# Kernel tuning notes

Hardware: AMD Instinct MI355X
Metric: run time of the kernel (lower is better)

The kernel has to match this reference:

```python
import jax, jax.numpy as jnp
import numpy as np

B = 16384
NEG = 10
V = 100000
E = 128

def setup_inputs() -> dict:
    key = jax.random.key(0)
    k1, k2, k3, k4, k5 = jax.random.split(key, 5)
    input_word = jax.random.randint(k1, (B,), 0, V)
    context_word = jax.random.randint(k2, (B,), 0, V)
    noise_words = jax.random.randint(k3, (B * NEG,), 0, V)
    # torch init: uniform_(-1, 1)
    W_in = jax.random.uniform(k4, (V, E), jnp.float32, -1.0, 1.0)
    W_ctx = jax.random.uniform(k5, (V, E), jnp.float32, -1.0, 1.0)
    return {"input_word": input_word, "context_word": context_word,
            "noise_words": noise_words, "W_in": W_in, "W_ctx": W_ctx}

def reference(input_word, context_word, noise_words, W_in, W_ctx):
    center = W_in[input_word]               # [B, E]
    ctx = W_ctx[context_word]               # [B, E]
    # positive score: per-example dot product
    out_loss = jax.nn.log_sigmoid(jnp.einsum('be,be->b', ctx, center))  # [B]
    noise = W_ctx[noise_words].reshape(B, NEG, E)                       # [B, NEG, E]
    # negative scores: -u_k . v_c
    neg_scores = -jnp.einsum('bke,be->bk', noise, center)               # [B, NEG]
    noise_loss = jax.nn.log_sigmoid(neg_scores).sum(axis=1)             # [B]
    return -(out_loss + noise_loss).mean()
```

## Files before the change

### kernel.cpp

```cpp
#include <hip/hip_runtime.h>
#include <hip/hip_bf16.h>

constexpr int kB   = 16384;
constexpr int kNeg = 10;
constexpr int kE   = 128;
constexpr int kWavesPerBlock = 4;
constexpr int kPairsPerWave  = 2;
constexpr int kBlocks = kB / (2 * kWavesPerBlock * kPairsPerWave);

__device__ __forceinline__ float log_sigmoid(float x) {
    return fminf(x, 0.0f) - log1pf(expf(-fabsf(x)));
}

__global__ __launch_bounds__(256) void w2v_loss_kernel(
    const int*   __restrict__ input_word,
    const int*   __restrict__ context_word,
    const int*   __restrict__ noise_words,
    const float* __restrict__ W_in,
    const float* __restrict__ W_ctx,
    float*       __restrict__ partials)
{
    const int lane = threadIdx.x & 63;
    const int wave = threadIdx.x >> 6;
    const int half = lane >> 5;
    const int l32  = lane & 31;

    const int wave_global = blockIdx.x * kWavesPerBlock + wave;
    const int pair0 = wave_global * kPairsPerWave;

    float acc = 0.0f;

    for (int p = 0; p < kPairsPerWave; ++p) {
        const int b = (pair0 + p) * 2 + half;
        if (b < kB) {
            const int iw = input_word[b];
            const int cw = context_word[b];
            const float4* __restrict__ crow = (const float4*)(W_in  + (size_t)iw * kE);
            const float4* __restrict__ xrow = (const float4*)(W_ctx + (size_t)cw * kE);
            const float4 c = crow[l32];
            const float4 x = xrow[l32];
            float pos = c.x * x.x + c.y * x.y + c.z * x.z + c.w * x.w;

            float negp[kNeg];
            #pragma unroll
            for (int k = 0; k < kNeg; ++k) {
                const int nw = noise_words[b * kNeg + k];
                const float4* __restrict__ nrow = (const float4*)(W_ctx + (size_t)nw * kE);
                const float4 nv = nrow[l32];
                negp[k] = c.x * nv.x + c.y * nv.y + c.z * nv.z + c.w * nv.w;
            }

            #pragma unroll
            for (int off = 16; off > 0; off >>= 1) {
                pos += __shfl_xor(pos, off);
                #pragma unroll
                for (int k = 0; k < kNeg; ++k)
                    negp[k] += __shfl_xor(negp[k], off);
            }

            if (l32 == 0) {
                float s = log_sigmoid(pos);
                #pragma unroll
                for (int k = 0; k < kNeg; ++k)
                    s += log_sigmoid(-negp[k]);
                acc += s;
            }
        }
    }

    #pragma unroll
    for (int off = 32; off > 0; off >>= 1)
        acc += __shfl_xor(acc, off);

    __shared__ float smem[kWavesPerBlock];
    if (lane == 0) smem[wave] = acc;
    __syncthreads();
    if (threadIdx.x == 0) {
        float t = 0.0f;
        #pragma unroll
        for (int w = 0; w < kWavesPerBlock; ++w) t += smem[w];
        partials[blockIdx.x] = t;
    }
}

__global__ __launch_bounds__(256) void w2v_reduce_kernel(
    const float* __restrict__ partials,
    float*       __restrict__ out)
{
    float acc = 0.0f;
    for (int i = threadIdx.x; i < kBlocks; i += 256)
        acc += partials[i];

    #pragma unroll
    for (int off = 32; off > 0; off >>= 1)
        acc += __shfl_xor(acc, off);

    __shared__ float smem[4];
    const int lane = threadIdx.x & 63;
    const int wave = threadIdx.x >> 6;
    if (lane == 0) smem[wave] = acc;
    __syncthreads();
    if (threadIdx.x == 0) {
        const float total = smem[0] + smem[1] + smem[2] + smem[3];
        out[0] = -total / (float)kB;
    }
}

extern "C" void kernel_launch(void* const* d_in, const int* in_sizes, int n_in,
                              void* d_out, int out_size, void* d_ws, size_t ws_size,
                              hipStream_t stream) {
    const int*   input_word   = (const int*)d_in[0];
    const int*   context_word = (const int*)d_in[1];
    const int*   noise_words  = (const int*)d_in[2];
    const float* W_in         = (const float*)d_in[3];
    const float* W_ctx        = (const float*)d_in[4];
    float*       out          = (float*)d_out;
    float*       partials     = (float*)d_ws;

    w2v_loss_kernel<<<kBlocks, 256, 0, stream>>>(
        input_word, context_word, noise_words, W_in, W_ctx, partials);
    w2v_reduce_kernel<<<1, 256, 0, stream>>>(partials, out);
}
```

Before: 134.0 us.

## Map four examples per wave with 16 lanes each and parallelize log-sigmoid

Restructures the work mapping so each wave handles four examples at once, with 16 lanes per example each loading two float4s per row, instead of looping over two pairs of examples with 32 lanes each. The per-example log-sigmoid evaluations are spread across lanes rather than computed serially by one lane. A minimum-blocks hint is added to launch bounds. The aim is more independent memory requests in flight per wave and less serial transcendental work, in exchange for more registers per lane and a shorter shuffle tree.

```diff
diff --git a/kernel.cpp b/kernel.cpp
--- a/kernel.cpp
+++ b/kernel.cpp
@@ -5,14 +5,18 @@
 constexpr int kNeg = 10;
 constexpr int kE   = 128;
 constexpr int kWavesPerBlock = 4;
-constexpr int kPairsPerWave  = 2;
-constexpr int kBlocks = kB / (2 * kWavesPerBlock * kPairsPerWave);
+constexpr int kExPerWave     = 4;
+constexpr int kBlocks = kB / (kWavesPerBlock * kExPerWave);
 
 __device__ __forceinline__ float log_sigmoid(float x) {
     return fminf(x, 0.0f) - log1pf(expf(-fabsf(x)));
 }
 
-__global__ __launch_bounds__(256) void w2v_loss_kernel(
+__device__ __forceinline__ float dot4(float4 a, float4 b) {
+    return a.x * b.x + a.y * b.y + a.z * b.z + a.w * b.w;
+}
+
+__global__ __launch_bounds__(256, 4) void w2v_loss_kernel(
     const int*   __restrict__ input_word,
     const int*   __restrict__ context_word,
     const int*   __restrict__ noise_words,
@@ -22,65 +26,57 @@
 {
     const int lane = threadIdx.x & 63;
     const int wave = threadIdx.x >> 6;
-    const int half = lane >> 5;
-    const int l32  = lane & 31;
+    const int l16  = lane & 15;
+    const int slot = lane >> 4;
 
     const int wave_global = blockIdx.x * kWavesPerBlock + wave;
-    const int pair0 = wave_global * kPairsPerWave;
+    const int b = wave_global * kExPerWave + slot;
 
-    float acc = 0.0f;
+    const int iw = input_word[b];
+    const int cw = context_word[b];
+    const float4* __restrict__ crow = (const float4*)(W_in  + (size_t)iw * kE);
+    const float4* __restrict__ xrow = (const float4*)(W_ctx + (size_t)cw * kE);
+    const float4 c0 = crow[l16];
+    const float4 c1 = crow[l16 + 16];
+    const float4 x0 = xrow[l16];
+    const float4 x1 = xrow[l16 + 16];
+    float pos = dot4(c0, x0) + dot4(c1, x1);
 
-    for (int p = 0; p < kPairsPerWave; ++p) {
-        const int b = (pair0 + p) * 2 + half;
-        if (b < kB) {
-            const int iw = input_word[b];
-            const int cw = context_word[b];
-            const float4* __restrict__ crow = (const float4*)(W_in  + (size_t)iw * kE);
-            const float4* __restrict__ xrow = (const float4*)(W_ctx + (size_t)cw * kE);
-            const float4 c = crow[l32];
-            const float4 x = xrow[l32];
-            float pos = c.x * x.x + c.y * x.y + c.z * x.z + c.w * x.w;
-
-            float negp[kNeg];
-            #pragma unroll
-            for (int k = 0; k < kNeg; ++k) {
-                const int nw = noise_words[b * kNeg + k];
-                const float4* __restrict__ nrow = (const float4*)(W_ctx + (size_t)nw * kE);
-                const float4 nv = nrow[l32];
-                negp[k] = c.x * nv.x + c.y * nv.y + c.z * nv.z + c.w * nv.w;
-            }
-
-            #pragma unroll
-            for (int off = 16; off > 0; off >>= 1) {
-                pos += __shfl_xor(pos, off);
-                #pragma unroll
-                for (int k = 0; k < kNeg; ++k)
-                    negp[k] += __shfl_xor(negp[k], off);
-            }
-
-            if (l32 == 0) {
-                float s = log_sigmoid(pos);
-                #pragma unroll
-                for (int k = 0; k < kNeg; ++k)
-                    s += log_sigmoid(-negp[k]);
-                acc += s;
-            }
-        }
+    float negp[kNeg];
+    #pragma unroll
+    for (int k = 0; k < kNeg; ++k) {
+        const int nw = noise_words[b * kNeg + k];
+        const float4* __restrict__ nrow = (const float4*)(W_ctx + (size_t)nw * kE);
+        const float4 n0 = nrow[l16];
+        const float4 n1 = nrow[l16 + 16];
+        negp[k] = dot4(c0, n0) + dot4(c1, n1);
     }
 
     #pragma unroll
-    for (int off = 32; off > 0; off >>= 1)
-        acc += __shfl_xor(acc, off);
+    for (int off = 8; off > 0; off >>= 1) {
+        pos += __shfl_xor(pos, off);
+        #pragma unroll
+        for (int k = 0; k < kNeg; ++k)
+            negp[k] += __shfl_xor(negp[k], off);
+    }
+
+    float v = pos;
+    #pragma unroll
+    for (int k = 0; k < kNeg; ++k)
+        v = (l16 == k + 1) ? -negp[k] : v;
+    float s = (l16 < 1 + kNeg) ? log_sigmoid(v) : 0.0f;
+
+    #pragma unroll
+    for (int off = 8; off > 0; off >>= 1)
+        s += __shfl_xor(s, off);
+    s += __shfl_xor(s, 16);
+    s += __shfl_xor(s, 32);
 
     __shared__ float smem[kWavesPerBlock];
-    if (lane == 0) smem[wave] = acc;
+    if (lane == 0) smem[wave] = s;
     __syncthreads();
-    if (threadIdx.x == 0) {
-        float t = 0.0f;
-        #pragma unroll
-        for (int w = 0; w < kWavesPerBlock; ++w) t += smem[w];
-        partials[blockIdx.x] = t;
-    }
+    if (threadIdx.x == 0)
+        partials[blockIdx.x] = smem[0] + smem[1] + smem[2] + smem[3];
 }
 
 __global__ __launch_bounds__(256) void w2v_reduce_kernel(
```

New measurement: 125.3 us. 1.07x faster.
